# Optimization experiments

Measured on AMD Instinct MI355X. Metric: run time of the kernel, lower is better.

## Reference

```python
import jax, jax.numpy as jnp
import numpy as np
from jax import lax

K = 3  # conv kernel size (causal)

def causal_conv1d(x, w, b):
    # x: [B, T, Cin], w: [K, Cin, Cout], b: [Cout]
    # TF 'causal' padding = pad left with (K-1) zeros.
    y = lax.conv_general_dilated(
        x, w,
        window_strides=(1,),
        padding=[(K - 1, 0)],
        dimension_numbers=("NWC", "WIO", "NWC"),
    )
    return y + b

def setup_inputs() -> dict:
    key = jax.random.key(0)
    ks = jax.random.split(key, 7)
    B, T, Cin, U = 8, 2048, 512, 512
    scale_in = 1.0 / np.sqrt(K * Cin)
    x = jax.random.normal(ks[0], (B, T, Cin), dtype=jnp.float32)
    Wq = jax.random.normal(ks[1], (K, Cin, U), dtype=jnp.float32) * scale_in
    Wk = jax.random.normal(ks[2], (K, Cin, U), dtype=jnp.float32) * scale_in
    Wv = jax.random.normal(ks[3], (K, Cin, U), dtype=jnp.float32) * scale_in
    bq = jnp.zeros((U,), dtype=jnp.float32)
    bk = jnp.zeros((U,), dtype=jnp.float32)
    bv = jnp.zeros((U,), dtype=jnp.float32)
    return {"x": x, "Wq": Wq, "bq": bq, "Wk": Wk, "bk": bk, "Wv": Wv, "bv": bv}

def reference(x, Wq, bq, Wk, bk, Wv, bv):
    # Self-attention path: query = key = value = x
    q = causal_conv1d(x, Wq, bq)   # [B, T, U]
    k = causal_conv1d(x, Wk, bk)   # [B, T, U]
    v = causal_conv1d(x, Wv, bv)   # [B, T, U]
    score = jnp.einsum("bqd,bkd->bqk", q, k)
    score = score / jnp.sqrt(jnp.asarray(v.shape[-1], dtype=score.dtype))
    # NOTE: faithful to source — softmax over axis=1 (the QUERY axis)
    score = jax.nn.softmax(score, axis=1)
    context = jnp.einsum("bqk,bkd->bqd", score, v)  # [B, T, U]
    return context
```

## Files before the change

### kernel.cpp

```cpp
#include <hip/hip_runtime.h>


#define B_   8
#define T_   2048
#define D_   512
#define KC_  1536
#define TPAD_ 2050

using short8   = __attribute__((ext_vector_type(8))) short;
using float4v  = __attribute__((ext_vector_type(4))) float;

__device__ __forceinline__ float bf2f(unsigned short b) {
  unsigned u = ((unsigned)b) << 16;
  float f; __builtin_memcpy(&f, &u, 4); return f;
}
__device__ __forceinline__ unsigned short f2bf(float f) {
  unsigned u; __builtin_memcpy(&u, &f, 4);
  u += 0x7fffu + ((u >> 16) & 1u);
  return (unsigned short)(u >> 16);
}

__device__ __forceinline__ void gld16(const void* g, void* l) {
  __builtin_amdgcn_global_load_lds((__attribute__((address_space(1))) void*)g,
                                   (__attribute__((address_space(3))) void*)l,
                                   16, 0, 0);
}

__device__ __forceinline__ float4v mfma16(short8 a, short8 b, float4v c) {
  return __builtin_amdgcn_mfma_f32_16x16x32_bf16(a, b, c, 0, 0, 0);
}

__global__ __launch_bounds__(256) void prep_x(const float* __restrict__ x,
                                              unsigned short* __restrict__ xpad) {
  const int b = blockIdx.y;
  const int i = (blockIdx.x * 256 + threadIdx.x) * 4;
  const int t = i >> 9;
  unsigned short* dst = xpad + (size_t)b * (TPAD_ * D_) + i;
  if (t < 2) {
    dst[0] = 0; dst[1] = 0; dst[2] = 0; dst[3] = 0;
  } else {
    const float* sp = x + ((size_t)b * T_ + (t - 2)) * D_ + (i & 511);
    float4v v = *(const float4v*)sp;
    dst[0] = f2bf(v[0]); dst[1] = f2bf(v[1]); dst[2] = f2bf(v[2]); dst[3] = f2bf(v[3]);
  }
}

__global__ __launch_bounds__(256) void concat_bias(const float* __restrict__ bq,
                                                   const float* __restrict__ bk,
                                                   const float* __restrict__ bv,
                                                   float* __restrict__ out) {
  const int i = blockIdx.x * 256 + threadIdx.x;
  float v = (i < 512) ? bq[i] : ((i < 1024) ? bk[i - 512] : bv[i - 1024]);
  out[i] = v;
}

__global__ __launch_bounds__(256) void transpose_w3(const float* __restrict__ Wq,
                                                    const float* __restrict__ Wk,
                                                    const float* __restrict__ Wv,
                                                    unsigned short* __restrict__ Wt) {
  __shared__ unsigned short tile[64][65];
  const float* s = (blockIdx.z == 0) ? Wq : (blockIdx.z == 1) ? Wk : Wv;
  unsigned short* d = Wt + (size_t)blockIdx.z * D_ * KC_;
  const int r0 = blockIdx.x * 64, c0 = blockIdx.y * 64;
  const int tc = threadIdx.x & 63, tg = threadIdx.x >> 6;
#pragma unroll
  for (int i = 0; i < 16; i++) {
    const int r = i * 4 + tg;
    tile[r][tc] = f2bf(s[(size_t)(r0 + r) * D_ + (c0 + tc)]);
  }
  __syncthreads();
#pragma unroll
  for (int i = 0; i < 16; i++) {
    const int rr = i * 4 + tg;
    d[(size_t)(c0 + rr) * KC_ + (r0 + tc)] = tile[tc][rr];
  }
}

__global__ __launch_bounds__(256) void transpose_v(const unsigned short* __restrict__ src,
                                                   unsigned short* __restrict__ dst) {
  __shared__ unsigned short tile[64][65];
  const unsigned short* s = src + (size_t)blockIdx.z * T_ * KC_;
  unsigned short* d = dst + (size_t)blockIdx.z * D_ * T_;
  const int r0 = blockIdx.x * 64, c0 = blockIdx.y * 64;
  const int tc = threadIdx.x & 63, tg = threadIdx.x >> 6;
#pragma unroll
  for (int i = 0; i < 16; i++) {
    const int r = i * 4 + tg;
    tile[r][tc] = s[(size_t)(r0 + r) * KC_ + (c0 + tc)];
  }
  __syncthreads();
#pragma unroll
  for (int i = 0; i < 16; i++) {
    const int rr = i * 4 + tg;
    d[(size_t)(c0 + rr) * T_ + (r0 + tc)] = tile[tc][rr];
  }
}

__global__ __launch_bounds__(256) void stats_combine(const float* __restrict__ pl,
                                                     long long sPz,
                                                     float* __restrict__ inv,
                                                     long long sIz) {
  const size_t z = blockIdx.z;
  const int col = blockIdx.x * 256 + threadIdx.x;
  float L = 0.f;
#pragma unroll
  for (int mb = 0; mb < 16; mb++)
    L += pl[z * (size_t)sPz + (size_t)mb * T_ + col];
  inv[z * (size_t)sIz + col] = 1.0f / L;
}

__global__ __launch_bounds__(256) void scale_vt(unsigned short* __restrict__ Vt,
                                                long long sVz,
                                                const float* __restrict__ inv,
                                                long long sIz) {
  const size_t z = blockIdx.z;
  unsigned short* Vb = Vt + z * (size_t)sVz;
  const float* iv = inv + z * (size_t)sIz;
  const int idx = (blockIdx.x * 256 + threadIdx.x) * 8;
  const int k = idx & (T_ - 1);
  short8 v = *(const short8*)(Vb + idx);
  float4v i0 = *(const float4v*)(iv + k);
  float4v i1 = *(const float4v*)(iv + k + 4);
  short8 o;
#pragma unroll
  for (int j = 0; j < 8; j++) {
    float s = (j < 4) ? i0[j & 3] : i1[j & 3];
    o[j] = (short)f2bf(bf2f((unsigned short)v[j]) * s);
  }
  *(short8*)(Vb + idx) = o;
}


#define RD_A(MH, BUF)                                                        \
  {                                                                          \
    const unsigned short* p_ =                                               \
        lds + (BUF) * 8192 + aoff + (MH) * (HFA * 1024);                     \
    _Pragma("unroll") for (int f_ = 0; f_ < HFA; ++f_) {                     \
      afr[MH][f_][0] = *(const short8*)(p_ + f_ * 1024 + q0);                \
      afr[MH][f_][1] = *(const short8*)(p_ + f_ * 1024 + q1);                \
    }                                                                        \
  }

#define RD_B(NH, BUF)                                                        \
  {                                                                          \
    const unsigned short* p_ =                                               \
        lds + 16384 + (BUF) * BLD + boff + (NH) * (HFB * 1024);              \
    _Pragma("unroll") for (int f_ = 0; f_ < HFB; ++f_) {                     \
      bfr[NH][f_][0] = *(const short8*)(p_ + f_ * 1024 + q0);                \
      bfr[NH][f_][1] = *(const short8*)(p_ + f_ * 1024 + q1);                \
    }                                                                        \
  }

#define MMA(MH, NH)                                                          \
  __builtin_amdgcn_s_setprio(1);                                             \
  _Pragma("unroll") for (int s_ = 0; s_ < 2; ++s_)                           \
  _Pragma("unroll") for (int f_ = 0; f_ < HFA; ++f_)                         \
  _Pragma("unroll") for (int g_ = 0; g_ < HFB; ++g_)                         \
      acc[(MH) * HFA + f_][(NH) * HFB + g_] =                                \
          mfma16(afr[MH][f_][s_], bfr[NH][g_][s_],                           \
                 acc[(MH) * HFA + f_][(NH) * HFB + g_]);                     \
  __builtin_amdgcn_s_setprio(0);

#define PH_MID                                                               \
  __builtin_amdgcn_s_barrier();                                              \
  asm volatile("s_waitcnt lgkmcnt(0)" ::: "memory");                         \
  __builtin_amdgcn_sched_barrier(0);

#define PH_END __builtin_amdgcn_s_barrier();

#define VMW                                                                  \
  do {                                                                       \
    if constexpr (GB == 6)                                                   \
      asm volatile("s_waitcnt vmcnt(6)" ::: "memory");                       \
    else                                                                     \
      asm volatile("s_waitcnt vmcnt(4)" ::: "memory");                       \
  } while (0)

template <int MODE, int BN>
__global__ __launch_bounds__(256, 2)
void gemm8(const unsigned short* __restrict__ A, long long sAz, int lda,
           const unsigned short* __restrict__ Bm, long long sBz, int ldb,
           void* __restrict__ Out, long long sOz, int ldo,
           const float* __restrict__ bias,
           float* __restrict__ pl, long long sPz,
           int Kdim, float scale) {
  constexpr int RW  = 64;
  constexpr int CW  = BN / 2;
  constexpr int FA  = 4;
  constexpr int FB  = CW / 16;
  constexpr int HFA = 2;
  constexpr int HFB = FB / 2;
  constexpr int GB  = BN / 32;
  constexpr int GBP2 = GB / 2;
  constexpr int BLD = BN * 64;
  __shared__ unsigned short lds[16384 + 2 * BLD];

  const int tid = threadIdx.x;
  const int l = tid & 63;
  const int wv = tid >> 6;
  const int wm = wv >> 1, wn = wv & 1;
  const int l15 = l & 15, hi = l >> 4, l7 = l & 7;
  const size_t z = blockIdx.z;
  const unsigned short* Ab = A + z * (size_t)sAz;
  const unsigned short* Bb = Bm + z * (size_t)sBz;
  const int m0 = blockIdx.x * 128, n0 = blockIdx.y * BN;
  const int NT = Kdim >> 6;
  const int NIT = NT >> 1;

  const int srow = tid >> 3;
  const int cswz = ((tid & 7) ^ ((tid >> 3) & 7)) << 3;
  const unsigned short* gA = Ab + (size_t)(m0 + srow) * lda + cswz;
  const unsigned short* gB = Bb + (size_t)(n0 + srow) * ldb + cswz;

  auto stgA = [&](int buf, int h, int kt) {
    if (kt >= NT) kt = NT - 1;
    unsigned short* d = lds + buf * 8192 + h * 4096 + tid * 8;
    const unsigned short* g = gA + (size_t)(h * 64) * lda + kt * 64;
    gld16(g, d);
    gld16(g + (size_t)32 * lda, d + 2048);
  };
  auto stgB = [&](int buf, int g, int kt) {
    if (kt >= NT) kt = NT - 1;
    unsigned short* d = lds + 16384 + buf * BLD + g * 2048 + tid * 8;
    const unsigned short* gp = gB + (size_t)(g * 32) * ldb + kt * 64;
    gld16(gp, d);
  };

  const int aoff = (wm * RW + l15) * 64;
  const int boff = (wn * CW + l15) * 64;
  const int q0 = ((0 + hi) ^ l7) << 3;
  const int q1 = ((4 + hi) ^ l7) << 3;

  short8 afr[2][HFA][2];
  short8 bfr[2][HFB][2];
  float4v acc[FA][FB];
#pragma unroll
  for (int i = 0; i < FA; ++i)
#pragma unroll
    for (int j = 0; j < FB; ++j)
#pragma unroll
      for (int r = 0; r < 4; ++r) acc[i][j][r] = 0.f;

#pragma unroll
  for (int g = 0; g < GB; ++g) stgB(0, g, 0);
  stgA(0, 0, 0); stgA(0, 1, 0);
#pragma unroll
  for (int g = 0; g < GB; ++g) stgB(1, g, 1);
  VMW;
  __builtin_amdgcn_s_barrier();
  __builtin_amdgcn_sched_barrier(0);

  for (int it = 0; it < NIT; ++it) {
    const int kt = 2 * it;
    RD_A(0, 0); RD_B(0, 0);
    stgA(1, 0, kt + 1);
    PH_MID; MMA(0, 0); PH_END;
    RD_B(1, 0);
    stgA(1, 1, kt + 1);
    PH_MID; MMA(0, 1); PH_END;
    RD_A(1, 0);
#pragma unroll
    for (int g = 0; g < GBP2; ++g) stgB(0, g, kt + 2);
    PH_MID; MMA(1, 1); PH_END;
#pragma unroll
    for (int g = GBP2; g < GB; ++g) stgB(0, g, kt + 2);
    PH_MID; MMA(1, 0); VMW; PH_END;
    RD_A(0, 1); RD_B(0, 1);
    stgA(0, 0, kt + 2);
    PH_MID; MMA(0, 0); PH_END;
    RD_B(1, 1);
    stgA(0, 1, kt + 2);
    PH_MID; MMA(0, 1); PH_END;
    RD_A(1, 1);
#pragma unroll
    for (int g = 0; g < GBP2; ++g) stgB(1, g, kt + 3);
    PH_MID; MMA(1, 1); PH_END;
#pragma unroll
    for (int g = GBP2; g < GB; ++g) stgB(1, g, kt + 3);
    PH_MID; MMA(1, 0); VMW; PH_END;
  }

  const int r0 = m0 + wm * RW + hi * 4;
  const int c0 = n0 + wn * CW + l15;

  if constexpr (MODE == 2) {
    float* O = (float*)Out + z * (size_t)sOz;
#pragma unroll
    for (int fm = 0; fm < FA; ++fm)
#pragma unroll
      for (int fn = 0; fn < FB; ++fn)
#pragma unroll
        for (int r = 0; r < 4; ++r)
          O[(size_t)(r0 + fm * 16 + r) * ldo + (c0 + fn * 16)] =
              acc[fm][fn][r] * scale;
  } else if constexpr (MODE == 0) {
    unsigned short* O = (unsigned short*)Out + z * (size_t)sOz;
#pragma unroll
    for (int fn = 0; fn < FB; ++fn) {
      const float badd = bias[c0 + fn * 16];
#pragma unroll
      for (int fm = 0; fm < FA; ++fm)
#pragma unroll
        for (int r = 0; r < 4; ++r)
          O[(size_t)(r0 + fm * 16 + r) * ldo + (c0 + fn * 16)] =
              f2bf(acc[fm][fn][r] * scale + badd);
    }
  } else {
    unsigned short* O = (unsigned short*)Out + z * (size_t)sOz;
    float cs[FB];
#pragma unroll
    for (int fn = 0; fn < FB; ++fn) cs[fn] = 0.f;
#pragma unroll
    for (int fm = 0; fm < FA; ++fm)
#pragma unroll
      for (int fn = 0; fn < FB; ++fn)
#pragma unroll
        for (int r = 0; r < 4; ++r) {
          float e = __expf(acc[fm][fn][r] * scale - 16.f);
          cs[fn] += e;
          O[(size_t)(r0 + fm * 16 + r) * ldo + (c0 + fn * 16)] = f2bf(e);
        }
#pragma unroll
    for (int fn = 0; fn < FB; ++fn) {
      cs[fn] += __shfl_xor(cs[fn], 16, 64);
      cs[fn] += __shfl_xor(cs[fn], 32, 64);
    }
    __syncthreads();
    float* red = (float*)(lds + 16384);
    if (hi == 0) {
#pragma unroll
      for (int fn = 0; fn < FB; ++fn)
        red[wm * BN + wn * CW + fn * 16 + l15] = cs[fn];
    }
    __syncthreads();
    if (tid < BN)
      pl[z * (size_t)sPz + (size_t)blockIdx.x * T_ + (n0 + tid)] =
          red[tid] + red[BN + tid];
  }
}

extern "C" void kernel_launch(void* const* d_in, const int* in_sizes, int n_in,
                              void* d_out, int out_size, void* d_ws, size_t ws_size,
                              hipStream_t stream) {
  const float* x  = (const float*)d_in[0];
  const float* Wq = (const float*)d_in[1];
  const float* bq = (const float*)d_in[2];
  const float* Wk = (const float*)d_in[3];
  const float* bk = (const float*)d_in[4];
  const float* Wv = (const float*)d_in[5];
  const float* bv = (const float*)d_in[6];

  char* ws = (char*)d_ws;
  auto alloc = [&](size_t bytes) {
    char* p = ws; ws += (bytes + 255) & ~(size_t)255; return p;
  };
  unsigned short* xpad = (unsigned short*)alloc((size_t)B_ * TPAD_ * D_ * 2);
  unsigned short* Wt   = (unsigned short*)alloc((size_t)KC_ * KC_ * 2);
  float*          bcat = (float*)alloc((size_t)KC_ * 4);
  unsigned short* QKV  = (unsigned short*)alloc((size_t)B_ * T_ * KC_ * 2);
  unsigned short* Vt   = (unsigned short*)alloc((size_t)B_ * D_ * T_ * 2);
  float* invb = (float*)alloc((size_t)B_ * T_ * 4);
  float* pl   = (float*)alloc((size_t)B_ * 16 * T_ * 4);
  size_t used = (size_t)(ws - (char*)d_ws);
  const size_t sAll = (size_t)B_ * T_ * T_ * 2;
  const size_t sOne = (size_t)T_ * T_ * 2;
  const int NB = (used + sAll <= ws_size) ? B_ : 1;
  unsigned short* Sb = (unsigned short*)alloc(NB == B_ ? sAll : sOne);

  prep_x<<<dim3(1025, B_), 256, 0, stream>>>(x, xpad);
  concat_bias<<<dim3(6), 256, 0, stream>>>(bq, bk, bv, bcat);
  transpose_w3<<<dim3(24, 8, 3), 256, 0, stream>>>(Wq, Wk, Wv, Wt);

  gemm8<0, 192><<<dim3(16, 8, B_), 256, 0, stream>>>(
      xpad, (long long)TPAD_ * D_, D_,
      Wt, 0, KC_,
      QKV, (long long)T_ * KC_, KC_,
      bcat, nullptr, 0, KC_, 1.0f);

  transpose_v<<<dim3(32, 8, B_), 256, 0, stream>>>(QKV + 2 * D_, Vt);

  const float scale = 0.044194173824159216f;
  for (int b0 = 0; b0 < B_; b0 += NB) {
    const unsigned short* Qp = QKV + (size_t)b0 * T_ * KC_;
    const unsigned short* Kp = QKV + (size_t)b0 * T_ * KC_ + D_;
    gemm8<1, 128><<<dim3(16, 16, NB), 256, 0, stream>>>(
        Qp, (long long)T_ * KC_, KC_,
        Kp, (long long)T_ * KC_, KC_,
        Sb, (long long)T_ * T_, T_,
        nullptr, pl + (size_t)b0 * 16 * T_, (long long)16 * T_,
        D_, scale);
    stats_combine<<<dim3(8, 1, NB), 256, 0, stream>>>(
        pl + (size_t)b0 * 16 * T_, (long long)16 * T_,
        invb + (size_t)b0 * T_, T_);
    scale_vt<<<dim3(512, 1, NB), 256, 0, stream>>>(
        Vt + (size_t)b0 * D_ * T_, (long long)D_ * T_,
        invb + (size_t)b0 * T_, T_);
    gemm8<2, 128><<<dim3(16, 4, NB), 256, 0, stream>>>(
        Sb, (long long)T_ * T_, T_,
        Vt + (size_t)b0 * D_ * T_, (long long)D_ * T_, T_,
        (float*)d_out + (size_t)b0 * T_ * D_, (long long)T_ * D_, D_,
        nullptr, nullptr, 0, T_, 1.0f);
  }
}
```

Measured before the change: 267.9 us.

## Stage GEMM epilogue through swizzled LDS, atomically accumulate column sums, merge small kernels

The MODE 0/1 GEMM epilogues now write bf16 results into a swizzled LDS tile and then store them to global memory as coalesced 16-byte rows, replacing scattered 2-byte stores. Column sums of the softmax exponentials are reduced with atomicAdd directly into a per-batch buffer that is zeroed by a memset, which removes the per-block partial-sum array and the stats_combine kernel. The reciprocal is folded into a new scale_vt2 kernel, and the bias concatenation is folded into transpose_w3, so fewer small kernels are launched. In exchange it adds a memset, float atomics whose summation order is nondeterministic, and LDS reuse in the epilogue that depends on the barrier placement.

```diff
diff --git a/kernel.cpp b/kernel.cpp
--- a/kernel.cpp
+++ b/kernel.cpp
@@ -45,24 +45,24 @@
   }
 }
 
-__global__ __launch_bounds__(256) void concat_bias(const float* __restrict__ bq,
-                                                   const float* __restrict__ bk,
-                                                   const float* __restrict__ bv,
-                                                   float* __restrict__ out) {
-  const int i = blockIdx.x * 256 + threadIdx.x;
-  float v = (i < 512) ? bq[i] : ((i < 1024) ? bk[i - 512] : bv[i - 1024]);
-  out[i] = v;
-}
-
 __global__ __launch_bounds__(256) void transpose_w3(const float* __restrict__ Wq,
                                                     const float* __restrict__ Wk,
                                                     const float* __restrict__ Wv,
-                                                    unsigned short* __restrict__ Wt) {
+                                                    unsigned short* __restrict__ Wt,
+                                                    const float* __restrict__ bq,
+                                                    const float* __restrict__ bk,
+                                                    const float* __restrict__ bv,
+                                                    float* __restrict__ bcat) {
   __shared__ unsigned short tile[64][65];
   const float* s = (blockIdx.z == 0) ? Wq : (blockIdx.z == 1) ? Wk : Wv;
   unsigned short* d = Wt + (size_t)blockIdx.z * D_ * KC_;
   const int r0 = blockIdx.x * 64, c0 = blockIdx.y * 64;
   const int tc = threadIdx.x & 63, tg = threadIdx.x >> 6;
+  if (blockIdx.x == 0 && blockIdx.y == 0) {
+    const float* bsrc = (blockIdx.z == 0) ? bq : (blockIdx.z == 1) ? bk : bv;
+    bcat[blockIdx.z * 512 + threadIdx.x] = bsrc[threadIdx.x];
+    bcat[blockIdx.z * 512 + 256 + threadIdx.x] = bsrc[256 + threadIdx.x];
+  }
 #pragma unroll
   for (int i = 0; i < 16; i++) {
     const int r = i * 4 + tg;
@@ -96,38 +96,30 @@
   }
 }
 
-__global__ __launch_bounds__(256) void stats_combine(const float* __restrict__ pl,
-                                                     long long sPz,
-                                                     float* __restrict__ inv,
-                                                     long long sIz) {
-  const size_t z = blockIdx.z;
-  const int col = blockIdx.x * 256 + threadIdx.x;
-  float L = 0.f;
-#pragma unroll
-  for (int mb = 0; mb < 16; mb++)
-    L += pl[z * (size_t)sPz + (size_t)mb * T_ + col];
-  inv[z * (size_t)sIz + col] = 1.0f / L;
-}
-
-__global__ __launch_bounds__(256) void scale_vt(unsigned short* __restrict__ Vt,
-                                                long long sVz,
-                                                const float* __restrict__ inv,
-                                                long long sIz) {
+__global__ __launch_bounds__(256) void scale_vt2(unsigned short* __restrict__ Vt,
+                                                 long long sVz,
+                                                 const float* __restrict__ pl,
+                                                 long long sPz) {
   const size_t z = blockIdx.z;
   unsigned short* Vb = Vt + z * (size_t)sVz;
-  const float* iv = inv + z * (size_t)sIz;
-  const int idx = (blockIdx.x * 256 + threadIdx.x) * 8;
-  const int k = idx & (T_ - 1);
-  short8 v = *(const short8*)(Vb + idx);
-  float4v i0 = *(const float4v*)(iv + k);
-  float4v i1 = *(const float4v*)(iv + k + 4);
-  short8 o;
-#pragma unroll
-  for (int j = 0; j < 8; j++) {
-    float s = (j < 4) ? i0[j & 3] : i1[j & 3];
-    o[j] = (short)f2bf(bf2f((unsigned short)v[j]) * s);
-  }
-  *(short8*)(Vb + idx) = o;
+  const float* Lz = pl + z * (size_t)sPz;
+  const int k0 = threadIdx.x * 8;
+  float4v a = *(const float4v*)(Lz + k0);
+  float4v b = *(const float4v*)(Lz + k0 + 4);
+  float inv[8];
+#pragma unroll
+  for (int j = 0; j < 4; j++) { inv[j] = 1.f / a[j]; inv[4 + j] = 1.f / b[j]; }
+  const int d0 = blockIdx.x * 8;
+#pragma unroll
+  for (int r = 0; r < 8; r++) {
+    unsigned short* p = Vb + (size_t)(d0 + r) * T_ + k0;
+    short8 v = *(const short8*)p;
+    short8 o;
+#pragma unroll
+    for (int j = 0; j < 8; j++)
+      o[j] = (short)f2bf(bf2f((unsigned short)v[j]) * inv[j]);
+    *(short8*)p = o;
+  }
 }
 
 
@@ -280,11 +272,11 @@
     PH_MID; MMA(1, 0); VMW; PH_END;
   }
 
-  const int r0 = m0 + wm * RW + hi * 4;
   const int c0 = n0 + wn * CW + l15;
 
   if constexpr (MODE == 2) {
     float* O = (float*)Out + z * (size_t)sOz;
+    const int r0 = m0 + wm * RW + hi * 4;
 #pragma unroll
     for (int fm = 0; fm < FA; ++fm)
 #pragma unroll
@@ -293,49 +285,53 @@
         for (int r = 0; r < 4; ++r)
           O[(size_t)(r0 + fm * 16 + r) * ldo + (c0 + fn * 16)] =
               acc[fm][fn][r] * scale;
-  } else if constexpr (MODE == 0) {
-    unsigned short* O = (unsigned short*)Out + z * (size_t)sOz;
-#pragma unroll
-    for (int fn = 0; fn < FB; ++fn) {
-      const float badd = bias[c0 + fn * 16];
-#pragma unroll
-      for (int fm = 0; fm < FA; ++fm)
-#pragma unroll
-        for (int r = 0; r < 4; ++r)
-          O[(size_t)(r0 + fm * 16 + r) * ldo + (c0 + fn * 16)] =
-              f2bf(acc[fm][fn][r] * scale + badd);
-    }
   } else {
-    unsigned short* O = (unsigned short*)Out + z * (size_t)sOz;
+    unsigned short* Plds = lds;
     float cs[FB];
 #pragma unroll
     for (int fn = 0; fn < FB; ++fn) cs[fn] = 0.f;
+    const int bc0 = (wn * CW) >> 3;
 #pragma unroll
     for (int fm = 0; fm < FA; ++fm)
 #pragma unroll
       for (int fn = 0; fn < FB; ++fn)
 #pragma unroll
         for (int r = 0; r < 4; ++r) {
-          float e = __expf(acc[fm][fn][r] * scale - 16.f);
-          cs[fn] += e;
-          O[(size_t)(r0 + fm * 16 + r) * ldo + (c0 + fn * 16)] = f2bf(e);
+          const int row = wm * RW + fm * 16 + hi * 4 + r;
+          const int cch = (bc0 + fn * 2 + (l15 >> 3)) ^ (row & 7);
+          float v = acc[fm][fn][r] * scale;
+          unsigned short h;
+          if constexpr (MODE == 1) {
+            float e = __expf(v - 16.f);
+            cs[fn] += e;
+            h = f2bf(e);
+          } else {
+            h = f2bf(v + bias[c0 + fn * 16]);
+          }
+          Plds[row * BN + (cch << 3) + (l15 & 7)] = h;
         }
-#pragma unroll
-    for (int fn = 0; fn < FB; ++fn) {
-      cs[fn] += __shfl_xor(cs[fn], 16, 64);
-      cs[fn] += __shfl_xor(cs[fn], 32, 64);
+    if constexpr (MODE == 1) {
+#pragma unroll
+      for (int fn = 0; fn < FB; ++fn) {
+        cs[fn] += __shfl_xor(cs[fn], 16, 64);
+        cs[fn] += __shfl_xor(cs[fn], 32, 64);
+      }
+      if (hi == 0) {
+#pragma unroll
+        for (int fn = 0; fn < FB; ++fn)
+          atomicAdd(&pl[z * (size_t)sPz + (n0 + wn * CW + fn * 16 + l15)],
+                    cs[fn]);
+      }
     }
     __syncthreads();
-    float* red = (float*)(lds + 16384);
-    if (hi == 0) {
-#pragma unroll
-      for (int fn = 0; fn < FB; ++fn)
-        red[wm * BN + wn * CW + fn * 16 + l15] = cs[fn];
+    unsigned short* O = (unsigned short*)Out + z * (size_t)sOz;
+    const int q = tid >> 1, half = tid & 1, q7 = (tid >> 1) & 7;
+#pragma unroll
+    for (int j = 0; j < BN / 16; ++j) {
+      const int cj = half * (BN / 16) + j;
+      short8 v = *(const short8*)&Plds[q * BN + ((cj ^ q7) << 3)];
+      *(short8*)&O[(size_t)(m0 + q) * ldo + n0 + cj * 8] = v;
     }
-    __syncthreads();
-    if (tid < BN)
-      pl[z * (size_t)sPz + (size_t)blockIdx.x * T_ + (n0 + tid)] =
-          red[tid] + red[BN + tid];
   }
 }
 
@@ -359,17 +355,17 @@
   float*          bcat = (float*)alloc((size_t)KC_ * 4);
   unsigned short* QKV  = (unsigned short*)alloc((size_t)B_ * T_ * KC_ * 2);
   unsigned short* Vt   = (unsigned short*)alloc((size_t)B_ * D_ * T_ * 2);
-  float* invb = (float*)alloc((size_t)B_ * T_ * 4);
-  float* pl   = (float*)alloc((size_t)B_ * 16 * T_ * 4);
+  float* pl   = (float*)alloc((size_t)B_ * T_ * 4);
   size_t used = (size_t)(ws - (char*)d_ws);
   const size_t sAll = (size_t)B_ * T_ * T_ * 2;
   const size_t sOne = (size_t)T_ * T_ * 2;
   const int NB = (used + sAll <= ws_size) ? B_ : 1;
   unsigned short* Sb = (unsigned short*)alloc(NB == B_ ? sAll : sOne);
 
+  hipMemsetAsync(pl, 0, (size_t)B_ * T_ * 4, stream);
   prep_x<<<dim3(1025, B_), 256, 0, stream>>>(x, xpad);
-  concat_bias<<<dim3(6), 256, 0, stream>>>(bq, bk, bv, bcat);
-  transpose_w3<<<dim3(24, 8, 3), 256, 0, stream>>>(Wq, Wk, Wv, Wt);
+  transpose_w3<<<dim3(24, 8, 3), 256, 0, stream>>>(Wq, Wk, Wv, Wt,
+                                                   bq, bk, bv, bcat);
 
   gemm8<0, 192><<<dim3(16, 8, B_), 256, 0, stream>>>(
       xpad, (long long)TPAD_ * D_, D_,
@@ -387,14 +383,11 @@
         Qp, (long long)T_ * KC_, KC_,
         Kp, (long long)T_ * KC_, KC_,
         Sb, (long long)T_ * T_, T_,
-        nullptr, pl + (size_t)b0 * 16 * T_, (long long)16 * T_,
+        nullptr, pl + (size_t)b0 * T_, (long long)T_,
         D_, scale);
-    stats_combine<<<dim3(8, 1, NB), 256, 0, stream>>>(
-        pl + (size_t)b0 * 16 * T_, (long long)16 * T_,
-        invb + (size_t)b0 * T_, T_);
-    scale_vt<<<dim3(512, 1, NB), 256, 0, stream>>>(
+    scale_vt2<<<dim3(64, 1, NB), 256, 0, stream>>>(
         Vt + (size_t)b0 * D_ * T_, (long long)D_ * T_,
-        invb + (size_t)b0 * T_, T_);
+        pl + (size_t)b0 * T_, (long long)T_);
     gemm8<2, 128><<<dim3(16, 4, NB), 256, 0, stream>>>(
         Sb, (long long)T_ * T_, T_,
         Vt + (size_t)b0 * D_ * T_, (long long)D_ * T_, T_,
```

Result: slower. 280.6 us (+4.7%).
